# Kernel tuning notes

Measured on AMD Instinct MI355X. Metric: run time of the kernel, lower is better.

Reference implementation:

```python
import jax, jax.numpy as jnp
import numpy as np

B, CIN, COUT, K, STRIDE, PAD = 32, 64, 128, 3, 1, 1
IN_H, IN_W = 112, 112


def setup_inputs() -> dict:
    key = jax.random.key(0)
    k1, k2 = jax.random.split(key)
    # x_padded already has `PAD` rows/cols of zeros on each side, as in the torch module
    x = jax.random.normal(k1, (B, CIN, IN_H, IN_W), dtype=jnp.float32)
    x_padded = jnp.pad(x, ((0, 0), (0, 0), (PAD, PAD), (PAD, PAD)))
    weight = jax.random.normal(k2, (COUT, CIN, K, K), dtype=jnp.float32) * 0.1
    bias = jnp.zeros((COUT,), dtype=jnp.float32)
    return {
        "x_padded": x_padded,
        "in_height": IN_H,
        "in_width": IN_W,
        "weight": weight,
        "bias": bias,
    }


def reference(x_padded, in_height, in_width, weight, bias):
    # CustomConv2D.custom_conv2d: direct conv over the pre-padded input.
    # out[b,o,h,w] = sum_{i,kh,kw} x_padded[b,i,h*s+kh,w*s+kw] * weight[o,i,kh,kw] + bias[o]
    out = jax.lax.conv_general_dilated(
        x_padded, weight,
        window_strides=(STRIDE, STRIDE),
        padding="VALID",  # padding already applied to x_padded
        dimension_numbers=("NCHW", "OIHW", "NCHW"),
    )
    return out + bias[None, :, None, None]
```

## Files before the change

### kernel.cpp

```cpp
#include <hip/hip_runtime.h>

typedef __attribute__((ext_vector_type(8))) short short8;
typedef __attribute__((ext_vector_type(4))) float f32x4;
typedef __attribute__((ext_vector_type(4))) unsigned int u32x4;
typedef unsigned short u16;
typedef unsigned int u32;
typedef unsigned long long u64;

#define XH 114
#define XW 114
#define CINC 64
#define COUT 128
#define OH 112
#define OW 112
#define NB 32
#define KTOT 576
#define TILEB 58368

static __device__ __forceinline__ u16 f2bf(float f) {
    u32 x = __float_as_uint(f);
    u32 r = (x + 0x7fffu + ((x >> 16) & 1u)) >> 16;
    return (u16)r;
}

#define MFMA16(a, b, c) __builtin_amdgcn_mfma_f32_16x16x32_bf16((a), (b), (c), 0, 0, 0)

static __device__ __forceinline__ void gload16(const void* g, void* l) {
    __builtin_amdgcn_global_load_lds(
        (const __attribute__((address_space(1))) unsigned int*)g,
        (__attribute__((address_space(3))) unsigned int*)l, 16, 0, 0);
}


__global__ __launch_bounds__(256) void wcvt_reord(const float* __restrict__ w,
                                                  u16* __restrict__ wbf) {
    int i = blockIdx.x * 256 + threadIdx.x;
    int o = i / KTOT;
    int rem = i - o * KTOT;
    int khkw = rem >> 6;
    int ci = rem & 63;
    wbf[i] = f2bf(w[(o * CINC + ci) * 9 + khkw]);
}

__global__ __launch_bounds__(256) void xcvt(const float* __restrict__ x,
                                            u16* __restrict__ xb) {
    __shared__ u16 tile[XW * 70];
    const int blk = blockIdx.x;
    const int b = blk / XH;
    const int h = blk - b * XH;
    const int tid = threadIdx.x;

    #pragma unroll
    for (int it = 0; it < 15; ++it) {
        int idx = it * 256 + tid;
        if (idx < 32 * XW) {
            int cp = idx / XW;
            int w_ = idx - cp * XW;
            const float* s0 = x + ((size_t)(b * CINC + 2 * cp) * XH + h) * XW + w_;
            float a = s0[0];
            float c = s0[XH * XW];
            u32 pk = (u32)f2bf(a) | ((u32)f2bf(c) << 16);
            *(u32*)&tile[w_ * 70 + 2 * cp] = pk;
        }
    }
    __syncthreads();

    u16* dstrow = xb + (size_t)(b * XH + h) * (XW * CINC);
    #pragma unroll
    for (int p2 = 0; p2 < 4; ++p2) {
        int task = p2 * 256 + tid;
        if (task < XW * 8) {
            int w_ = task >> 3;
            int c8 = task & 7;
            const u32* s = (const u32*)&tile[w_ * 70 + c8 * 8];
            u32x4 v = {s[0], s[1], s[2], s[3]};
            int slot = c8 ^ ((2 * h + w_) & 7);
            *(u32x4*)(dstrow + w_ * CINC + slot * 8) = v;
        }
    }
}

__global__ __launch_bounds__(512, 2) void conv_pers(const u16* __restrict__ xb,
                                                    const u16* __restrict__ wbf,
                                                    const float* __restrict__ bias,
                                                    float* __restrict__ out) {
    __shared__ u16 lds[2 * 4 * XW * CINC];
    char* ldsc = (char*)lds;

    const int tid  = threadIdx.x;
    const int lane = tid & 63;
    const int wv   = tid >> 6;
    const int l16  = lane & 15;
    const int lhi  = lane >> 4;
    const int wm   = wv & 3;
    const int wn   = wv >> 2;

    const int t0g = blockIdx.x * 7;

    const u16* wrow0 = wbf + (wm * 32 + l16) * KTOT + lhi * 8;
    const u16* wrow1 = wrow0 + 16 * KTOT;
    short8 areg[18][2];
    #pragma unroll
    for (int t = 0; t < 18; ++t) {
        areg[t][0] = *(const short8*)(wrow0 + t * 32);
        areg[t][1] = *(const short8*)(wrow1 + t * 32);
    }

    {
        const char* src = (const char*)(xb + (size_t)((t0g / 56) * XH + (t0g % 56) * 2) * (XW * CINC));
        #pragma unroll
        for (int it = 0; it < 8; ++it) {
            int off = it * 8192 + wv * 1024;
            if (off < TILEB) gload16(src + off + lane * 16, ldsc + off);
        }
    }

    const f32x4 zero = {0.f, 0.f, 0.f, 0.f};

    #pragma unroll 1
    for (int i = 0; i < 7; ++i) {
        __syncthreads();

        if (i < 6) {
            const int tg = t0g + i + 1;
            const char* src = (const char*)(xb + (size_t)((tg / 56) * XH + (tg % 56) * 2) * (XW * CINC));
            char* dstb = ldsc + ((i + 1) & 1) * TILEB;
            #pragma unroll
            for (int it = 0; it < 8; ++it) {
                int off = it * 8192 + wv * 1024;
                if (off < TILEB) gload16(src + off + lane * 16, dstb + off);
            }
        }

        const int tg = t0g + i;
        const int b  = tg / 56;
        const int h0 = (tg - b * 56) * 2;
        char* buf = ldsc + (i & 1) * TILEB;

        f32x4 acc[2][7];
        #pragma unroll
        for (int mf = 0; mf < 2; ++mf)
            #pragma unroll
            for (int nf = 0; nf < 7; ++nf) acc[mf][nf] = zero;

        #pragma unroll
        for (int tt = 0; tt < 9; ++tt) {
            const int kh = tt / 3;
            const int kw = tt - kh * 3;
            const int r  = wn + kh;
            const int pix0 = r * XW + kw + l16;
            const int hash = (2 * (h0 + r) + kw + l16) & 7;
            const int ba0 = (pix0 << 7) + ((lhi ^ hash) << 4);

            __builtin_amdgcn_s_setprio(1);
            #pragma unroll
            for (int nf = 0; nf < 7; ++nf) {
                short8 bf = *(const short8*)(buf + ba0 + nf * 2048);
                acc[0][nf] = MFMA16(areg[2 * tt][0], bf, acc[0][nf]);
                acc[1][nf] = MFMA16(areg[2 * tt][1], bf, acc[1][nf]);
            }
            __builtin_amdgcn_s_setprio(0);

            __builtin_amdgcn_s_setprio(1);
            #pragma unroll
            for (int nf = 0; nf < 7; ++nf) {
                short8 bf = *(const short8*)(buf + (ba0 ^ 0x40) + nf * 2048);
                acc[0][nf] = MFMA16(areg[2 * tt + 1][0], bf, acc[0][nf]);
                acc[1][nf] = MFMA16(areg[2 * tt + 1][1], bf, acc[1][nf]);
            }
            __builtin_amdgcn_s_setprio(0);
        }

        float* outb = out + (size_t)b * COUT * (OH * OW) + (h0 + wn) * OW;
        #pragma unroll
        for (int mf = 0; mf < 2; ++mf) {
            #pragma unroll
            for (int j = 0; j < 4; ++j) {
                const int o = wm * 32 + mf * 16 + lhi * 4 + j;
                const float bv = bias[o];
                #pragma unroll
                for (int nf = 0; nf < 7; ++nf) {
                    outb[(size_t)o * (OH * OW) + nf * 16 + l16] = acc[mf][nf][j] + bv;
                }
            }
        }
    }
}


#define BK 32
#define NSTEP 18
#define LDB 40

__global__ __launch_bounds__(256) void wcvt_ident(const float* __restrict__ w,
                                                  u16* __restrict__ wbf) {
    int i = blockIdx.x * 256 + threadIdx.x;
    if (i < COUT * KTOT) wbf[i] = f2bf(w[i]);
}

__global__ __launch_bounds__(256) void conv_fb(const float* __restrict__ x,
                                               const u16* __restrict__ wbf,
                                               const float* __restrict__ bias,
                                               float* __restrict__ out) {
    __shared__ u16 ldsB[OW * LDB];
    const int tid = threadIdx.x;
    int bid = blockIdx.x;
    { int xcd = bid & 7; bid = xcd * 448 + (bid >> 3); }
    const int b = bid / OH;
    const int h = bid - b * OH;
    const float* xbp = x + (size_t)b * (CINC * XH * XW);
    float* outb = out + (size_t)b * (COUT * OH * OW) + h * OW;
    const int lane = tid & 63, wv = tid >> 6, l16 = lane & 15, lhi = lane >> 4;
    const int m0 = wv * 32;
    const int sk = tid >> 3, sn0 = (tid & 7) * 14;
    f32x4 acc[2][7];
    const f32x4 zero = {0.f, 0.f, 0.f, 0.f};
    #pragma unroll
    for (int i = 0; i < 2; ++i)
        #pragma unroll
        for (int j = 0; j < 7; ++j) acc[i][j] = zero;
    for (int t = 0; t < NSTEP; ++t) {
        const int kg = t * BK + sk;
        const int ci = kg / 9;
        const int r9 = kg - ci * 9;
        const int kh = r9 / 3, kw = r9 - (r9 / 3) * 3;
        const float* src = xbp + ((size_t)ci * XH + (h + kh)) * XW + kw + sn0;
        __syncthreads();
        #pragma unroll
        for (int i = 0; i < 14; ++i) ldsB[(sn0 + i) * LDB + sk] = f2bf(src[i]);
        __syncthreads();
        short8 afrag[2];
        #pragma unroll
        for (int mf = 0; mf < 2; ++mf)
            afrag[mf] = *(const short8*)(wbf + (m0 + mf * 16 + l16) * KTOT + t * BK + lhi * 8);
        #pragma unroll
        for (int nf = 0; nf < 7; ++nf) {
            short8 bfrag = *(const short8*)&ldsB[(nf * 16 + l16) * LDB + lhi * 8];
            acc[0][nf] = MFMA16(afrag[0], bfrag, acc[0][nf]);
            acc[1][nf] = MFMA16(afrag[1], bfrag, acc[1][nf]);
        }
    }
    #pragma unroll
    for (int mf = 0; mf < 2; ++mf)
        #pragma unroll
        for (int j = 0; j < 4; ++j) {
            const int o = m0 + mf * 16 + lhi * 4 + j;
            const float bv = bias[o];
            #pragma unroll
            for (int nf = 0; nf < 7; ++nf)
                outb[(size_t)o * (OH * OW) + nf * 16 + l16] = acc[mf][nf][j] + bv;
        }
}

extern "C" void kernel_launch(void* const* d_in, const int* in_sizes, int n_in,
                              void* d_out, int out_size, void* d_ws, size_t ws_size,
                              hipStream_t stream) {
    const float* x    = (const float*)d_in[0];
    const float* w    = (const float*)d_in[3];
    const float* bias = (const float*)d_in[4];
    float* out = (float*)d_out;

    const size_t WBYTES = (size_t)COUT * KTOT * 2;
    const size_t XBYTES = (size_t)NB * XH * XW * CINC * 2;
    if (ws_size >= WBYTES + XBYTES) {
        u16* wbf = (u16*)d_ws;
        u16* xb  = (u16*)((char*)d_ws + WBYTES);
        wcvt_reord<<<(COUT * KTOT) / 256, 256, 0, stream>>>(w, wbf);
        xcvt<<<NB * XH, 256, 0, stream>>>(x, xb);
        conv_pers<<<256, 512, 0, stream>>>(xb, wbf, bias, out);
    } else {
        u16* wbf = (u16*)d_ws;
        wcvt_ident<<<(COUT * KTOT + 255) / 256, 256, 0, stream>>>(w, wbf);
        conv_fb<<<NB * OH, 256, 0, stream>>>(x, wbf, bias, out);
    }
}
```

Measured before the change: 122.1 us.

## Merge prep kernels, transpose MFMA operands for vector stores, remap blocks across XCDs

The weight-reorder and input-convert kernels are merged into one prep launch, which saves a kernel launch. In the conv kernel the MFMA operand order is swapped so each lane holds four consecutive output pixels, which allows 16-byte vectorized stores with the bias hoisted into registers. Block indices are remapped so consecutive tiles land on the same XCD. The loop-top barrier is replaced by a manual waitcnt plus s_barrier at the loop end. The hand-written vmcnt(14) wait is fragile: it relies on exact counts of outstanding loads and stores being correct for the prefetch.

After: 120.9 us. Within noise of the previous version (-1.0%).

```diff
diff --git a/kernel.cpp b/kernel.cpp
--- a/kernel.cpp
+++ b/kernel.cpp
@@ -5,7 +5,6 @@
 typedef __attribute__((ext_vector_type(4))) unsigned int u32x4;
 typedef unsigned short u16;
 typedef unsigned int u32;
-typedef unsigned long long u64;
 
 #define XH 114
 #define XW 114
@@ -32,23 +31,24 @@
 }
 
 
-__global__ __launch_bounds__(256) void wcvt_reord(const float* __restrict__ w,
-                                                  u16* __restrict__ wbf) {
-    int i = blockIdx.x * 256 + threadIdx.x;
-    int o = i / KTOT;
-    int rem = i - o * KTOT;
-    int khkw = rem >> 6;
-    int ci = rem & 63;
-    wbf[i] = f2bf(w[(o * CINC + ci) * 9 + khkw]);
-}
-
-__global__ __launch_bounds__(256) void xcvt(const float* __restrict__ x,
-                                            u16* __restrict__ xb) {
+__global__ __launch_bounds__(256) void prep(const float* __restrict__ x,
+                                            const float* __restrict__ w,
+                                            u16* __restrict__ xb,
+                                            u16* __restrict__ wbf) {
+    const int tid = threadIdx.x;
+    const int blk = blockIdx.x;
+    if (blk >= NB * XH) {
+        int i = (blk - NB * XH) * 256 + tid;
+        int o = i / KTOT;
+        int rem = i - o * KTOT;
+        int khkw = rem >> 6;
+        int ci = rem & 63;
+        wbf[i] = f2bf(w[(o * CINC + ci) * 9 + khkw]);
+        return;
+    }
     __shared__ u16 tile[XW * 70];
-    const int blk = blockIdx.x;
     const int b = blk / XH;
     const int h = blk - b * XH;
-    const int tid = threadIdx.x;
 
     #pragma unroll
     for (int it = 0; it < 15; ++it) {
@@ -80,10 +80,10 @@
     }
 }
 
-__global__ __launch_bounds__(512, 2) void conv_pers(const u16* __restrict__ xb,
-                                                    const u16* __restrict__ wbf,
-                                                    const float* __restrict__ bias,
-                                                    float* __restrict__ out) {
+__global__ __launch_bounds__(512, 2) void conv_pers2(const u16* __restrict__ xb,
+                                                     const u16* __restrict__ wbf,
+                                                     const float* __restrict__ bias,
+                                                     float* __restrict__ out) {
     __shared__ u16 lds[2 * 4 * XW * CINC];
     char* ldsc = (char*)lds;
 
@@ -95,7 +95,9 @@
     const int wm   = wv & 3;
     const int wn   = wv >> 2;
 
-    const int t0g = blockIdx.x * 7;
+    int bidx = blockIdx.x;
+    { int xcd = bidx & 7; bidx = xcd * 32 + (bidx >> 3); }
+    const int t0g = bidx * 7;
 
     const u16* wrow0 = wbf + (wm * 32 + l16) * KTOT + lhi * 8;
     const u16* wrow1 = wrow0 + 16 * KTOT;
@@ -105,22 +107,24 @@
         areg[t][0] = *(const short8*)(wrow0 + t * 32);
         areg[t][1] = *(const short8*)(wrow1 + t * 32);
     }
+    const float bv0 = bias[wm * 32 + l16];
+    const float bv1 = bias[wm * 32 + 16 + l16];
 
     {
-        const char* src = (const char*)(xb + (size_t)((t0g / 56) * XH + (t0g % 56) * 2) * (XW * CINC));
+        const int tg = t0g;
+        const char* src = (const char*)(xb + (size_t)((tg / 56) * XH + (tg % 56) * 2) * (XW * CINC));
         #pragma unroll
         for (int it = 0; it < 8; ++it) {
             int off = it * 8192 + wv * 1024;
             if (off < TILEB) gload16(src + off + lane * 16, ldsc + off);
         }
     }
+    __syncthreads();
 
     const f32x4 zero = {0.f, 0.f, 0.f, 0.f};
 
     #pragma unroll 1
     for (int i = 0; i < 7; ++i) {
-        __syncthreads();
-
         if (i < 6) {
             const int tg = t0g + i + 1;
             const char* src = (const char*)(xb + (size_t)((tg / 56) * XH + (tg % 56) * 2) * (XW * CINC));
@@ -133,8 +137,8 @@
         }
 
         const int tg = t0g + i;
-        const int b  = tg / 56;
-        const int h0 = (tg - b * 56) * 2;
+        const int bb  = tg / 56;
+        const int hh0 = (tg - bb * 56) * 2;
         char* buf = ldsc + (i & 1) * TILEB;
 
         f32x4 acc[2][7];
@@ -149,15 +153,15 @@
             const int kw = tt - kh * 3;
             const int r  = wn + kh;
             const int pix0 = r * XW + kw + l16;
-            const int hash = (2 * (h0 + r) + kw + l16) & 7;
+            const int hash = (2 * (hh0 + r) + kw + l16) & 7;
             const int ba0 = (pix0 << 7) + ((lhi ^ hash) << 4);
 
             __builtin_amdgcn_s_setprio(1);
             #pragma unroll
             for (int nf = 0; nf < 7; ++nf) {
                 short8 bf = *(const short8*)(buf + ba0 + nf * 2048);
-                acc[0][nf] = MFMA16(areg[2 * tt][0], bf, acc[0][nf]);
-                acc[1][nf] = MFMA16(areg[2 * tt][1], bf, acc[1][nf]);
+                acc[0][nf] = MFMA16(bf, areg[2 * tt][0], acc[0][nf]);
+                acc[1][nf] = MFMA16(bf, areg[2 * tt][1], acc[1][nf]);
             }
             __builtin_amdgcn_s_setprio(0);
 
@@ -165,25 +169,29 @@
             #pragma unroll
             for (int nf = 0; nf < 7; ++nf) {
                 short8 bf = *(const short8*)(buf + (ba0 ^ 0x40) + nf * 2048);
-                acc[0][nf] = MFMA16(areg[2 * tt + 1][0], bf, acc[0][nf]);
-                acc[1][nf] = MFMA16(areg[2 * tt + 1][1], bf, acc[1][nf]);
+                acc[0][nf] = MFMA16(bf, areg[2 * tt + 1][0], acc[0][nf]);
+                acc[1][nf] = MFMA16(bf, areg[2 * tt + 1][1], acc[1][nf]);
             }
             __builtin_amdgcn_s_setprio(0);
         }
 
-        float* outb = out + (size_t)b * COUT * (OH * OW) + (h0 + wn) * OW;
         #pragma unroll
         for (int mf = 0; mf < 2; ++mf) {
-            #pragma unroll
-            for (int j = 0; j < 4; ++j) {
-                const int o = wm * 32 + mf * 16 + lhi * 4 + j;
-                const float bv = bias[o];
-                #pragma unroll
-                for (int nf = 0; nf < 7; ++nf) {
-                    outb[(size_t)o * (OH * OW) + nf * 16 + l16] = acc[mf][nf][j] + bv;
-                }
-            }
-        }
+            const int o = wm * 32 + mf * 16 + l16;
+            const float bv = mf ? bv1 : bv0;
+            float* po = out + ((size_t)bb * COUT + o) * (OH * OW) + (hh0 + wn) * OW;
+            #pragma unroll
+            for (int nf = 0; nf < 7; ++nf) {
+                f32x4 v = acc[mf][nf];
+                v[0] += bv; v[1] += bv; v[2] += bv; v[3] += bv;
+                *(f32x4*)(po + nf * 16 + lhi * 4) = v;
+            }
+        }
+
+        __builtin_amdgcn_sched_barrier(0);
+        asm volatile("s_waitcnt vmcnt(14) lgkmcnt(0)" ::: "memory");
+        __builtin_amdgcn_sched_barrier(0);
+        __builtin_amdgcn_s_barrier();
     }
 }
 
@@ -265,9 +273,8 @@
     if (ws_size >= WBYTES + XBYTES) {
         u16* wbf = (u16*)d_ws;
         u16* xb  = (u16*)((char*)d_ws + WBYTES);
-        wcvt_reord<<<(COUT * KTOT) / 256, 256, 0, stream>>>(w, wbf);
-        xcvt<<<NB * XH, 256, 0, stream>>>(x, xb);
-        conv_pers<<<256, 512, 0, stream>>>(xb, wbf, bias, out);
+        prep<<<NB * XH + (COUT * KTOT) / 256, 256, 0, stream>>>(x, w, xb, wbf);
+        conv_pers2<<<256, 512, 0, stream>>>(xb, wbf, bias, out);
     } else {
         u16* wbf = (u16*)d_ws;
         wcvt_ident<<<(COUT * KTOT + 255) / 256, 256, 0, stream>>>(w, wbf);
```
